# Performance work log

Hardware: AMD Instinct MI355X
Metric: run time of the kernel (lower is better)

Reference implementation:

```python
import jax, jax.numpy as jnp
import numpy as np

N = 50000   # nodes
E = 800000  # edges before self-loops
H = 4       # heads
D = 64      # num_h_feats (per-head out dim of hidden layers)
C = 2       # num_classes
NEG = 0.2   # DGL GATConv leaky_relu negative_slope
EPS = 1e-5  # BatchNorm eps


def setup_inputs() -> dict:
    key = jax.random.key(0)
    ks = jax.random.split(key, 16)
    inp = {}
    inp['feats'] = jax.random.normal(ks[0], (N, 9), jnp.float32)
    inp['W1'] = jax.random.normal(ks[1], (9, H * D), jnp.float32) * 0.1
    inp['al1'] = jax.random.normal(ks[2], (H, D), jnp.float32) * 0.1
    inp['ar1'] = jax.random.normal(ks[3], (H, D), jnp.float32) * 0.1
    inp['b1'] = jnp.zeros((H, D), jnp.float32)
    inp['Wm'] = jax.random.normal(ks[4], (D, H * D), jnp.float32) * 0.1
    inp['alm'] = jax.random.normal(ks[5], (H, D), jnp.float32) * 0.1
    inp['arm'] = jax.random.normal(ks[6], (H, D), jnp.float32) * 0.1
    inp['bm'] = jnp.zeros((H, D), jnp.float32)
    inp['W2'] = jax.random.normal(ks[7], (D, H * C), jnp.float32) * 0.1
    inp['al2'] = jax.random.normal(ks[8], (H, C), jnp.float32) * 0.1
    inp['ar2'] = jax.random.normal(ks[9], (H, C), jnp.float32) * 0.1
    inp['b2'] = jnp.zeros((H, C), jnp.float32)
    inp['gamma'] = jnp.ones((D,), jnp.float32)
    inp['beta'] = jnp.zeros((D,), jnp.float32)
    inp['src'] = jax.random.randint(ks[10], (E,), 0, N, jnp.int32)
    inp['dst'] = jax.random.randint(ks[11], (E,), 0, N, jnp.int32)
    return inp


def gat_layer(x, W, al, ar, b, src, dst, out_d):
    """DGL GATConv: linear -> per-edge attention -> dst-softmax -> scatter-sum."""
    n = x.shape[0]
    z = (x @ W).reshape(n, H, out_d)                 # [N, H, Dout]
    el = jnp.sum(z * al, axis=-1)                    # [N, H] attn on src
    er = jnp.sum(z * ar, axis=-1)                    # [N, H] attn on dst
    e = jax.nn.leaky_relu(el[src] + er[dst], NEG)    # [E, H]
    m = jax.ops.segment_max(e, dst, num_segments=n)  # per-dst max (stable softmax)
    a = jnp.exp(e - m[dst])
    s = jax.ops.segment_sum(a, dst, num_segments=n)
    alpha = a / s[dst]                               # [E, H]
    out = jax.ops.segment_sum(alpha[:, :, None] * z[src], dst, num_segments=n)
    return out + b                                   # [N, H, Dout]


def batchnorm(h, gamma, beta):
    mu = jnp.mean(h, axis=0)
    var = jnp.var(h, axis=0)
    return (h - mu) * jax.lax.rsqrt(var + EPS) * gamma + beta


def reference(feats, W1, al1, ar1, b1, Wm, alm, arm, bm, W2, al2, ar2, b2,
              gamma, beta, src, dst):
    # dgl.add_self_loop
    loop = jnp.arange(N, dtype=src.dtype)
    s = jnp.concatenate([src, loop])
    d = jnp.concatenate([dst, loop])
    h = gat_layer(feats, W1, al1, ar1, b1, s, d, D).sum(axis=1)  # head-sum
    h = batchnorm(h, gamma, beta)
    h = gat_layer(h, Wm, alm, arm, bm, s, d, D).sum(axis=1)
    h = batchnorm(h, gamma, beta)
    o = gat_layer(h, W2, al2, ar2, b2, s, d, C).sum(axis=1)      # [N, C]
    return o
```

## Files before the change

kernel.cpp:

```cpp
#include <hip/hip_runtime.h>
#include <hip/hip_bf16.h>

typedef __hip_bfloat16 bf16;
typedef __bf16 bf16x8 __attribute__((ext_vector_type(8)));
typedef float f32x4 __attribute__((ext_vector_type(4)));
typedef _Float16 h16;
typedef _Float16 h16x4 __attribute__((ext_vector_type(4)));

#define LOG2E 1.44269504088896340736f

__device__ __forceinline__ float b2f(bf16 v) { return __bfloat162float(v); }

__device__ __forceinline__ float ldin(const void* p, size_t i, int isb) {
    return isb ? b2f(((const bf16*)p)[i]) : ((const float*)p)[i];
}
__device__ __forceinline__ unsigned short f2bfbits(float f) {
    bf16 v = __float2bfloat16(f);
    return *(unsigned short*)&v;
}

__global__ __launch_bounds__(256) void prep_kernel(
    const void* __restrict__ feats, const void* __restrict__ W1, const void* __restrict__ Wm,
    const void* __restrict__ al1, const void* __restrict__ ar1,
    const void* __restrict__ alm, const void* __restrict__ arm,
    const unsigned* __restrict__ gbits,
    unsigned short* __restrict__ fpad, unsigned short* __restrict__ W1T,
    unsigned short* __restrict__ WmT,
    float* __restrict__ alf1, float* __restrict__ arf1,
    float* __restrict__ alfm, float* __restrict__ arfm,
    unsigned short* __restrict__ zhs, float* __restrict__ zcs, float* __restrict__ elp,
    int* __restrict__ flag, int Nn) {
    int isb = (gbits[0] == 0x3F803F80u) ? 1 : 0;
    long t = (long)blockIdx.x * 256 + threadIdx.x;
    if (t == 0) *flag = isb;
    long n64 = (long)Nn * 64;
    if (t < n64) {
        int k = (int)(t & 63); long n = t >> 6;
        fpad[t] = (k < 9) ? f2bfbits(ldin(feats, (size_t)n * 9 + k, isb)) : 0;
    } else if (t < n64 + 16384) {
        long u = t - n64; int n = (int)(u >> 6), k = (int)(u & 63);
        W1T[u] = (k < 9) ? f2bfbits(ldin(W1, (size_t)k * 256 + n, isb)) : 0;
    } else if (t < n64 + 32768) {
        long u = t - n64 - 16384; int n = (int)(u >> 6), k = (int)(u & 63);
        WmT[u] = f2bfbits(ldin(Wm, (size_t)k * 256 + n, isb));
    } else if (t < n64 + 32768 + 256) {
        int u = (int)(t - n64 - 32768);
        alf1[u] = ldin(al1, u, isb) * LOG2E; arf1[u] = ldin(ar1, u, isb) * LOG2E;
        alfm[u] = ldin(alm, u, isb) * LOG2E; arfm[u] = ldin(arm, u, isb) * LOG2E;
    } else {
        long u = t - (n64 + 32768 + 256);
        if (u < 4) {
            elp[(size_t)Nn * 4 + u] = -1e30f;
        } else if (u < 260) {
            zhs[(size_t)Nn * 256 + (u - 4)] = 0;
        } else if (u < 268) {
            zcs[(size_t)Nn * 8 + (u - 260)] = 0.f;
        }
    }
}

__global__ __launch_bounds__(256) void count_kernel(
    const int* __restrict__ dst, int* __restrict__ deg, int E) {
    int t = blockIdx.x * 256 + threadIdx.x;
    if (t < E) atomicAdd(&deg[dst[t]], 1);
}

__global__ __launch_bounds__(256) void scan1_kernel(
    const int* __restrict__ deg, int* __restrict__ off, int* __restrict__ bsum, int Nn) {
    __shared__ int s[256];
    int t = threadIdx.x, i = blockIdx.x * 256 + t;
    int v = (i < Nn) ? deg[i] : 0;
    s[t] = v; __syncthreads();
#pragma unroll
    for (int o = 1; o < 256; o <<= 1) {
        int a = (t >= o) ? s[t - o] : 0;
        __syncthreads();
        s[t] += a;
        __syncthreads();
    }
    if (i < Nn) off[i] = s[t];
    if (t == 255) bsum[blockIdx.x] = s[255];
}

__global__ __launch_bounds__(256) void scan2_kernel(int* __restrict__ bsum, int NB) {
    __shared__ int s[256];
    int t = threadIdx.x;
    int v = (t < NB) ? bsum[t] : 0;
    s[t] = v; __syncthreads();
#pragma unroll
    for (int o = 1; o < 256; o <<= 1) {
        int a = (t >= o) ? s[t - o] : 0;
        __syncthreads();
        s[t] += a;
        __syncthreads();
    }
    if (t < NB) bsum[t] = s[t] - v;
}

__global__ __launch_bounds__(256) void scan3_kernel(
    const int* __restrict__ deg, int* __restrict__ off, int* __restrict__ cur,
    const int* __restrict__ bsum, int Nn, int E) {
    int i = blockIdx.x * 256 + threadIdx.x;
    if (i < Nn) {
        int ex = off[i] - deg[i] + bsum[i >> 8];
        off[i] = ex;
        cur[i] = ex;
    }
    if (i == 0) off[Nn] = E;
}

__global__ __launch_bounds__(256) void scatter_kernel(
    const int* __restrict__ src, const int* __restrict__ dst,
    int* __restrict__ cur, int* __restrict__ adj, int E) {
    int t = blockIdx.x * 256 + threadIdx.x;
    if (t < E) {
        int p = atomicAdd(&cur[dst[t]], 1);
        adj[p] = src[t];
    }
}

__global__ __launch_bounds__(256) void lin_mfma_l1_kernel(
    const unsigned short* __restrict__ xb, const unsigned short* __restrict__ WT,
    const float* __restrict__ alf, const float* __restrict__ arf,
    h16* __restrict__ zh, float* __restrict__ el, float* __restrict__ er, int Nn) {
    __shared__ h16 zs[16 * 256];
    int w = threadIdx.x >> 6;
    int l = threadIdx.x & 63;
    int quad = l >> 4, lc = l & 15;
    int node0 = blockIdx.x * 16;

    int mrow = node0 + lc; if (mrow >= Nn) mrow = Nn - 1;
    const bf16x8* xa = (const bf16x8*)(xb + (size_t)mrow * 64);
    bf16x8 a0 = xa[quad];
    bf16x8 a1 = xa[quad + 4];

    float pe[4] = {0.f, 0.f, 0.f, 0.f}, pr[4] = {0.f, 0.f, 0.f, 0.f};
    int row0 = quad * 4;
#pragma unroll
    for (int ct = 0; ct < 4; ++ct) {
        int col = w * 64 + ct * 16 + lc;
        const bf16x8* wb = (const bf16x8*)(WT + (size_t)col * 64);
        bf16x8 b0 = wb[quad];
        bf16x8 b1 = wb[quad + 4];
        f32x4 c = {0.f, 0.f, 0.f, 0.f};
        c = __builtin_amdgcn_mfma_f32_16x16x32_bf16(a0, b0, c, 0, 0, 0);
        c = __builtin_amdgcn_mfma_f32_16x16x32_bf16(a1, b1, c, 0, 0, 0);
        float av = alf[col], rv = arf[col];
#pragma unroll
        for (int r = 0; r < 4; ++r) {
            pe[r] = fmaf(c[r], av, pe[r]);
            pr[r] = fmaf(c[r], rv, pr[r]);
            zs[(row0 + r) * 256 + col] = (h16)c[r];
        }
    }
#pragma unroll
    for (int o = 1; o < 16; o <<= 1) {
#pragma unroll
        for (int r = 0; r < 4; ++r) {
            pe[r] += __shfl_xor(pe[r], o);
            pr[r] += __shfl_xor(pr[r], o);
        }
    }
    if (lc == 0) {
#pragma unroll
        for (int r = 0; r < 4; ++r) {
            int n = node0 + row0 + r;
            if (n < Nn) { el[n * 4 + w] = pe[r]; er[n * 4 + w] = pr[r]; }
        }
    }
    __syncthreads();
#pragma unroll
    for (int it = 0; it < 2; ++it) {
        int flat = it * 2048 + threadIdx.x * 8;
        int row = flat >> 8;
        if (node0 + row < Nn)
            *(uint4*)(zh + (size_t)node0 * 256 + flat) = *(const uint4*)(zs + flat);
    }
}

__global__ __launch_bounds__(256) void lin_mfma_bn_kernel(
    const float* __restrict__ x, const float* __restrict__ sc, const float* __restrict__ shb,
    const unsigned short* __restrict__ WT,
    const float* __restrict__ alf, const float* __restrict__ arf,
    h16* __restrict__ zh, float* __restrict__ el, float* __restrict__ er, int Nn) {
    __shared__ h16 zs[16 * 256];
    int w = threadIdx.x >> 6;
    int l = threadIdx.x & 63;
    int quad = l >> 4, lc = l & 15;
    int node0 = blockIdx.x * 16;

    int mrow = node0 + lc; if (mrow >= Nn) mrow = Nn - 1;
    const float* xr = x + (size_t)mrow * 64 + quad * 8;
    float4 f0 = ((const float4*)xr)[0];
    float4 f1 = ((const float4*)xr)[1];
    float4 f2 = ((const float4*)(xr + 32))[0];
    float4 f3 = ((const float4*)(xr + 32))[1];
    float4 s0 = ((const float4*)(sc + quad * 8))[0];
    float4 s1 = ((const float4*)(sc + quad * 8))[1];
    float4 s2 = ((const float4*)(sc + 32 + quad * 8))[0];
    float4 s3 = ((const float4*)(sc + 32 + quad * 8))[1];
    float4 h0 = ((const float4*)(shb + quad * 8))[0];
    float4 h1 = ((const float4*)(shb + quad * 8))[1];
    float4 h2 = ((const float4*)(shb + 32 + quad * 8))[0];
    float4 h3 = ((const float4*)(shb + 32 + quad * 8))[1];

    union { bf16x8 v; unsigned short s[8]; } ua, ub;
    ua.s[0] = f2bfbits(fmaf(f0.x, s0.x, h0.x));
    ua.s[1] = f2bfbits(fmaf(f0.y, s0.y, h0.y));
    ua.s[2] = f2bfbits(fmaf(f0.z, s0.z, h0.z));
    ua.s[3] = f2bfbits(fmaf(f0.w, s0.w, h0.w));
    ua.s[4] = f2bfbits(fmaf(f1.x, s1.x, h1.x));
    ua.s[5] = f2bfbits(fmaf(f1.y, s1.y, h1.y));
    ua.s[6] = f2bfbits(fmaf(f1.z, s1.z, h1.z));
    ua.s[7] = f2bfbits(fmaf(f1.w, s1.w, h1.w));
    ub.s[0] = f2bfbits(fmaf(f2.x, s2.x, h2.x));
    ub.s[1] = f2bfbits(fmaf(f2.y, s2.y, h2.y));
    ub.s[2] = f2bfbits(fmaf(f2.z, s2.z, h2.z));
    ub.s[3] = f2bfbits(fmaf(f2.w, s2.w, h2.w));
    ub.s[4] = f2bfbits(fmaf(f3.x, s3.x, h3.x));
    ub.s[5] = f2bfbits(fmaf(f3.y, s3.y, h3.y));
    ub.s[6] = f2bfbits(fmaf(f3.z, s3.z, h3.z));
    ub.s[7] = f2bfbits(fmaf(f3.w, s3.w, h3.w));
    bf16x8 a0 = ua.v, a1 = ub.v;

    float pe[4] = {0.f, 0.f, 0.f, 0.f}, pr[4] = {0.f, 0.f, 0.f, 0.f};
    int row0 = quad * 4;
#pragma unroll
    for (int ct = 0; ct < 4; ++ct) {
        int col = w * 64 + ct * 16 + lc;
        const bf16x8* wb = (const bf16x8*)(WT + (size_t)col * 64);
        bf16x8 b0 = wb[quad];
        bf16x8 b1 = wb[quad + 4];
        f32x4 c = {0.f, 0.f, 0.f, 0.f};
        c = __builtin_amdgcn_mfma_f32_16x16x32_bf16(a0, b0, c, 0, 0, 0);
        c = __builtin_amdgcn_mfma_f32_16x16x32_bf16(a1, b1, c, 0, 0, 0);
        float av = alf[col], rv = arf[col];
#pragma unroll
        for (int r = 0; r < 4; ++r) {
            pe[r] = fmaf(c[r], av, pe[r]);
            pr[r] = fmaf(c[r], rv, pr[r]);
            zs[(row0 + r) * 256 + col] = (h16)c[r];
        }
    }
#pragma unroll
    for (int o = 1; o < 16; o <<= 1) {
#pragma unroll
        for (int r = 0; r < 4; ++r) {
            pe[r] += __shfl_xor(pe[r], o);
            pr[r] += __shfl_xor(pr[r], o);
        }
    }
    if (lc == 0) {
#pragma unroll
        for (int r = 0; r < 4; ++r) {
            int n = node0 + row0 + r;
            if (n < Nn) { el[n * 4 + w] = pe[r]; er[n * 4 + w] = pr[r]; }
        }
    }
    __syncthreads();
#pragma unroll
    for (int it = 0; it < 2; ++it) {
        int flat = it * 2048 + threadIdx.x * 8;
        int row = flat >> 8;
        if (node0 + row < Nn)
            *(uint4*)(zh + (size_t)node0 * 256 + flat) = *(const uint4*)(zs + flat);
    }
}

__global__ __launch_bounds__(256) void bnstats_kernel(
    const float* __restrict__ x, float* __restrict__ bnsum, float* __restrict__ bnsumsq,
    int Nn) {
    __shared__ float ssum[4][64], ssq[4][64];
    int tid = threadIdx.x;
    int d = tid & 63, r = tid >> 6;
    float s = 0.f, q = 0.f;
    int stride = gridDim.x * 4;
    for (int n = blockIdx.x * 4 + r; n < Nn; n += stride) {
        float v = x[(size_t)n * 64 + d];
        s += v;
        q = fmaf(v, v, q);
    }
    ssum[r][d] = s; ssq[r][d] = q;
    __syncthreads();
    if (tid < 64) {
        float ts = ssum[0][tid] + ssum[1][tid] + ssum[2][tid] + ssum[3][tid];
        float tq = ssq[0][tid] + ssq[1][tid] + ssq[2][tid] + ssq[3][tid];
        atomicAdd(&bnsum[tid], ts);
        atomicAdd(&bnsumsq[tid], tq);
    }
}

__global__ void bn_coef_kernel(
    const float* __restrict__ bnsum, const float* __restrict__ bnsumsq,
    const void* __restrict__ gamma, const void* __restrict__ beta,
    float* __restrict__ sc, float* __restrict__ shb,
    const int* __restrict__ flag, int Nn) {
    int isb = *flag;
    int d = threadIdx.x;
    if (d >= 64) return;
    float inv_n = 1.f / (float)Nn;
    float mu = bnsum[d] * inv_n;
    float var = bnsumsq[d] * inv_n - mu * mu;
    float s = rsqrtf(var + 1e-5f) * ldin(gamma, d, isb);
    sc[d] = s;
    shb[d] = ldin(beta, d, isb) - mu * s;
}

__global__ __launch_bounds__(256) void lin3_kernel(
    const float* __restrict__ x, const float* __restrict__ sc, const float* __restrict__ shb,
    const void* __restrict__ W, const void* __restrict__ al, const void* __restrict__ ar,
    float* __restrict__ zc, float* __restrict__ el, float* __restrict__ er,
    const int* __restrict__ flag, int Nn) {
    int isb = *flag;
    int t = blockIdx.x * 256 + threadIdx.x;
    if (t >= Nn * 4) return;
    int n = t >> 2, h = t & 3;
    const float* xr = x + (size_t)n * 64;
    float a0 = 0.f, a1 = 0.f;
#pragma unroll 8
    for (int k = 0; k < 64; k++) {
        float xn = fmaf(xr[k], sc[k], shb[k]);
        a0 += xn * ldin(W, k * 8 + h * 2 + 0, isb);
        a1 += xn * ldin(W, k * 8 + h * 2 + 1, isb);
    }
    zc[n * 8 + h * 2 + 0] = a0;
    zc[n * 8 + h * 2 + 1] = a1;
    el[t] = (a0 * ldin(al, h * 2, isb) + a1 * ldin(al, h * 2 + 1, isb)) * LOG2E;
    er[t] = (a0 * ldin(ar, h * 2, isb) + a1 * ldin(ar, h * 2 + 1, isb)) * LOG2E;
}

#define LDADJ(dstv, bidx)                                   \
    {                                                       \
        _Pragma("unroll") for (int j = 0; j < 4; j++) {     \
            int idx = (bidx) + j;                           \
            int ok = idx < s1;                              \
            int v = adj[ok ? idx : s0];                     \
            dstv[j] = ok ? v : Nn;                          \
        }                                                   \
    }
#define ISSUE(ev, zv, ss)                                                          \
    {                                                                              \
        _Pragma("unroll") for (int j = 0; j < 4; j++) ev[j] = el[ss[j] * 4 + h];   \
        _Pragma("unroll") for (int j = 0; j < 4; j++)                              \
            zv[j] = zrow[(size_t)ss[j] * 64 + l];                                  \
    }
#define COMPUTE(ev, zv)                                     \
    {                                                       \
        _Pragma("unroll") for (int j = 0; j < 4; j++) {     \
            float e = ev[j] + ern;                          \
            e = fmaxf(e, 0.2f * e);                         \
            float wj = __builtin_amdgcn_exp2f(e);           \
            lsum += wj;                                     \
            acc.x = fmaf(wj, (float)zv[j].x, acc.x);        \
            acc.y = fmaf(wj, (float)zv[j].y, acc.y);        \
            acc.z = fmaf(wj, (float)zv[j].z, acc.z);        \
            acc.w = fmaf(wj, (float)zv[j].w, acc.w);        \
        }                                                   \
    }

__global__ __launch_bounds__(256) void gat_agg64_kernel(
    const h16* __restrict__ zh, const float* __restrict__ el, const float* __restrict__ er,
    const int* __restrict__ off, const int* __restrict__ adj, const void* __restrict__ bias,
    float* __restrict__ x, const int* __restrict__ flag, int Nn, int total_waves) {
    int isb = *flag;
    int tid = threadIdx.x;
    int l = tid & 63;
    int h = l >> 4;
    int gw = blockIdx.x * 4 + (tid >> 6);
    const h16x4* zrow = (const h16x4*)zh;

    float4 bsl;
    bsl.x = ldin(bias, l * 4 + 0, isb);
    bsl.y = ldin(bias, l * 4 + 1, isb);
    bsl.z = ldin(bias, l * 4 + 2, isb);
    bsl.w = ldin(bias, l * 4 + 3, isb);

    if (gw >= Nn) return;

    int n = gw;
    int fs0 = off[n], fs1 = off[n + 1];
    float fel = el[n * 4 + h], fer = er[n * 4 + h];

    while (true) {
        int s0 = fs0, s1 = fs1;
        float eln = fel, ern = fer;
        h16x4 zself = zrow[(size_t)n * 64 + l];
        int nn = n + total_waves;
        if (nn < Nn) {
            fs0 = off[nn]; fs1 = off[nn + 1];
            fel = el[nn * 4 + h]; fer = er[nn * 4 + h];
        }

        float e0 = eln + ern;
        e0 = fmaxf(e0, 0.2f * e0);
        float w0 = __builtin_amdgcn_exp2f(e0);
        float lsum = w0;
        float4 acc = {0.f, 0.f, 0.f, 0.f};

        int deg = s1 - s0;
        if (deg > 0) {
            int nb = (deg + 3) >> 2;
            int sA[4], sB[4];
            float evA[4], evB[4];
            h16x4 zvA[4], zvB[4];
            LDADJ(sA, s0);
            ISSUE(evA, zvA, sA);
            if (nb > 1) LDADJ(sB, s0 + 4);
            int k = 0;
            while (true) {
                if (k + 1 < nb) ISSUE(evB, zvB, sB);
                if (k + 2 < nb) LDADJ(sA, s0 + (k + 2) * 4);
                COMPUTE(evA, zvA);
                if (++k >= nb) break;
                if (k + 1 < nb) ISSUE(evA, zvA, sA);
                if (k + 2 < nb) LDADJ(sB, s0 + (k + 2) * 4);
                COMPUTE(evB, zvB);
                if (++k >= nb) break;
            }
        }

        acc.x = fmaf(w0, (float)zself.x, acc.x);
        acc.y = fmaf(w0, (float)zself.y, acc.y);
        acc.z = fmaf(w0, (float)zself.z, acc.z);
        acc.w = fmaf(w0, (float)zself.w, acc.w);

        float inv = 1.f / lsum;
        float4 r;
        r.x = fmaf(acc.x, inv, bsl.x);
        r.y = fmaf(acc.y, inv, bsl.y);
        r.z = fmaf(acc.z, inv, bsl.z);
        r.w = fmaf(acc.w, inv, bsl.w);
#pragma unroll
        for (int o = 16; o < 64; o <<= 1) {
            r.x += __shfl_xor(r.x, o);
            r.y += __shfl_xor(r.y, o);
            r.z += __shfl_xor(r.z, o);
            r.w += __shfl_xor(r.w, o);
        }
        if (h == 0) ((float4*)(x + (size_t)n * 64))[l & 15] = r;
        if (nn >= Nn) break;
        n = nn;
    }
}
#undef LDADJ
#undef ISSUE
#undef COMPUTE

__global__ __launch_bounds__(256) void gat_agg2_kernel(
    const float* __restrict__ zc, const float* __restrict__ el, const float* __restrict__ er,
    const int* __restrict__ off, const int* __restrict__ adj, const void* __restrict__ bias,
    void* __restrict__ out, const int* __restrict__ flag, int Nn) {
    int isb = *flag;
    int t = blockIdx.x * 256 + threadIdx.x;
    if (t >= Nn * 4) return;
    int n = t >> 2, h = t & 3;
    float er_nh = er[n * 4 + h];
    float e0 = el[n * 4 + h] + er_nh;
    e0 = fmaxf(e0, 0.2f * e0);
    float w0 = __builtin_amdgcn_exp2f(e0);
    float lsum = w0;
    float2 zn = ((const float2*)zc)[n * 4 + h];
    float a0 = w0 * zn.x, a1 = w0 * zn.y;
    int s0 = off[n], s1 = off[n + 1];
    for (int i = s0; i < s1; i += 4) {
        int ss[4];
#pragma unroll
        for (int j = 0; j < 4; j++) {
            int idx = i + j;
            int ok = idx < s1;
            int v = adj[ok ? idx : s0];
            ss[j] = ok ? v : Nn;
        }
        float ev[4]; float2 zj[4];
#pragma unroll
        for (int j = 0; j < 4; j++) {
            ev[j] = el[ss[j] * 4 + h];
            zj[j] = ((const float2*)zc)[ss[j] * 4 + h];
        }
#pragma unroll
        for (int j = 0; j < 4; j++) {
            float e = ev[j] + er_nh;
            e = fmaxf(e, 0.2f * e);
            float w = __builtin_amdgcn_exp2f(e);
            lsum += w;
            a0 = fmaf(w, zj[j].x, a0);
            a1 = fmaf(w, zj[j].y, a1);
        }
    }
    float inv = 1.f / lsum;
    float v0 = fmaf(a0, inv, ldin(bias, h * 2 + 0, isb));
    float v1 = fmaf(a1, inv, ldin(bias, h * 2 + 1, isb));
#pragma unroll
    for (int o = 1; o < 4; o <<= 1) {
        v0 += __shfl_xor(v0, o);
        v1 += __shfl_xor(v1, o);
    }
    if (h == 0) {
        if (isb) {
            ((bf16*)out)[n * 2 + 0] = __float2bfloat16(v0);
            ((bf16*)out)[n * 2 + 1] = __float2bfloat16(v1);
        } else {
            ((float*)out)[n * 2 + 0] = v0;
            ((float*)out)[n * 2 + 1] = v1;
        }
    }
}

extern "C" void kernel_launch(void* const* d_in, const int* in_sizes, int n_in,
                              void* d_out, int out_size, void* d_ws, size_t ws_size,
                              hipStream_t stream) {
    const void* feats = d_in[0];
    const void* W1    = d_in[1];
    const void* al1   = d_in[2];
    const void* ar1   = d_in[3];
    const void* b1    = d_in[4];
    const void* Wm    = d_in[5];
    const void* alm   = d_in[6];
    const void* arm   = d_in[7];
    const void* bm    = d_in[8];
    const void* W2    = d_in[9];
    const void* al2   = d_in[10];
    const void* ar2   = d_in[11];
    const void* b2v   = d_in[12];
    const void* gamma = d_in[13];
    const void* beta  = d_in[14];
    const int*  src   = (const int*)d_in[15];
    const int*  dst   = (const int*)d_in[16];

    int Nn = in_sizes[0] / 9;
    int E  = in_sizes[15];

    float* ws = (float*)d_ws;
    h16*   zh   = (h16*)ws;
    float* zc   = ws + (size_t)Nn * 128 + 128;
    float* el   = zc + (size_t)Nn * 8 + 8;
    float* er   = el + (size_t)Nn * 4 + 4;
    float* x    = er + (size_t)Nn * 4;
    int*   deg  = (int*)(x + (size_t)Nn * 64);
    float* bns1 = (float*)(deg + Nn);
    float* bnq1 = bns1 + 64;
    float* bns2 = bnq1 + 64;
    float* bnq2 = bns2 + 64;
    size_t msetBytes = (size_t)Nn * 4 + 256 * 4;
    float* sc1  = bnq2 + 64;
    float* shb1 = sc1 + 64;
    float* sc2  = shb1 + 64;
    float* shb2 = sc2 + 64;
    float* alf1 = shb2 + 64;
    float* arf1 = alf1 + 256;
    float* alfm = arf1 + 256;
    float* arfm = alfm + 256;
    unsigned short* fpad = (unsigned short*)(arfm + 256);
    unsigned short* W1T  = fpad + (size_t)Nn * 64;
    unsigned short* WmT  = W1T + 256 * 64;
    int*   flag = (int*)(WmT + 256 * 64);
    int*   off  = flag + 1;
    int*   cur  = off + Nn + 1;
    int*   adj  = cur + Nn;
    int*   bsum = adj + E;

    dim3 B(256);
    int NB1 = (Nn + 255) / 256;
    int gE  = (E + 255) / 256;
    int gMF = (Nn + 15) / 16;
    int gN4 = (Nn * 4 + 255) / 256;
    long prepN = (long)Nn * 64 + 32768 + 256 + 268;
    int gPrep = (int)((prepN + 255) / 256);
    int AGG_GRID = 2048;
    int total_waves = AGG_GRID * 4;

    prep_kernel<<<gPrep, B, 0, stream>>>(feats, W1, Wm, al1, ar1, alm, arm,
                                         (const unsigned*)gamma, fpad, W1T, WmT,
                                         alf1, arf1, alfm, arfm,
                                         (unsigned short*)zh, zc, el, flag, Nn);

    hipMemsetAsync(deg, 0, msetBytes, stream);
    count_kernel<<<gE, B, 0, stream>>>(dst, deg, E);
    scan1_kernel<<<NB1, B, 0, stream>>>(deg, off, bsum, Nn);
    scan2_kernel<<<1, B, 0, stream>>>(bsum, NB1);
    scan3_kernel<<<NB1, B, 0, stream>>>(deg, off, cur, bsum, Nn, E);
    scatter_kernel<<<gE, B, 0, stream>>>(src, dst, cur, adj, E);

    lin_mfma_l1_kernel<<<gMF, B, 0, stream>>>(fpad, W1T, alf1, arf1, zh, el, er, Nn);
    gat_agg64_kernel<<<AGG_GRID, B, 0, stream>>>(
        zh, el, er, off, adj, b1, x, flag, Nn, total_waves);
    bnstats_kernel<<<512, B, 0, stream>>>(x, bns1, bnq1, Nn);
    bn_coef_kernel<<<1, 64, 0, stream>>>(bns1, bnq1, gamma, beta, sc1, shb1, flag, Nn);

    lin_mfma_bn_kernel<<<gMF, B, 0, stream>>>(x, sc1, shb1, WmT, alfm, arfm, zh, el, er, Nn);
    gat_agg64_kernel<<<AGG_GRID, B, 0, stream>>>(
        zh, el, er, off, adj, bm, x, flag, Nn, total_waves);
    bnstats_kernel<<<512, B, 0, stream>>>(x, bns2, bnq2, Nn);
    bn_coef_kernel<<<1, 64, 0, stream>>>(bns2, bnq2, gamma, beta, sc2, shb2, flag, Nn);

    lin3_kernel<<<gN4, B, 0, stream>>>(x, sc2, shb2, W2, al2, ar2, zc, el, er, flag, Nn);
    gat_agg2_kernel<<<gN4, B, 0, stream>>>(zc, el, er, off, adj, b2v, d_out, flag, Nn);
}
```

Before: 465.2 us.

## Fuse CSR build and BN coef into neighbors; pad adjacency to 4 for vector loads

Folds the degree count into the prep kernel and replaces the three-kernel scan with a single-block scan that pads each node's neighbor list to a multiple of 4, using sentinel entries that point at the padding node. The aggregation kernels then read neighbors with aligned int4 loads and no bounds masks. BN coefficient computation moves into the consuming linear kernels, and the prep kernel writes 16-byte vectors. This removes several small launches and per-edge masking, at the cost of a serial single-block scan over 50k nodes and some padded edge work.

```diff
diff --git a/kernel.cpp b/kernel.cpp
--- a/kernel.cpp
+++ b/kernel.cpp
@@ -24,53 +24,84 @@
     const void* __restrict__ al1, const void* __restrict__ ar1,
     const void* __restrict__ alm, const void* __restrict__ arm,
     const unsigned* __restrict__ gbits,
+    const int* __restrict__ dstv, int* __restrict__ deg,
     unsigned short* __restrict__ fpad, unsigned short* __restrict__ W1T,
     unsigned short* __restrict__ WmT,
     float* __restrict__ alf1, float* __restrict__ arf1,
     float* __restrict__ alfm, float* __restrict__ arfm,
     unsigned short* __restrict__ zhs, float* __restrict__ zcs, float* __restrict__ elp,
-    int* __restrict__ flag, int Nn) {
+    int* __restrict__ flag, int Nn, int E) {
     int isb = (gbits[0] == 0x3F803F80u) ? 1 : 0;
     long t = (long)blockIdx.x * 256 + threadIdx.x;
     if (t == 0) *flag = isb;
-    long n64 = (long)Nn * 64;
-    if (t < n64) {
-        int k = (int)(t & 63); long n = t >> 6;
-        fpad[t] = (k < 9) ? f2bfbits(ldin(feats, (size_t)n * 9 + k, isb)) : 0;
-    } else if (t < n64 + 16384) {
-        long u = t - n64; int n = (int)(u >> 6), k = (int)(u & 63);
-        W1T[u] = (k < 9) ? f2bfbits(ldin(W1, (size_t)k * 256 + n, isb)) : 0;
-    } else if (t < n64 + 32768) {
-        long u = t - n64 - 16384; int n = (int)(u >> 6), k = (int)(u & 63);
-        WmT[u] = f2bfbits(ldin(Wm, (size_t)k * 256 + n, isb));
-    } else if (t < n64 + 32768 + 256) {
-        int u = (int)(t - n64 - 32768);
+    long b0 = (long)Nn * 8;
+    long b1 = b0 + 2048;
+    long b2 = b1 + 2048;
+    long b3 = b2 + 256;
+    long b4 = b3 + 268;
+    long b5 = b4 + E;
+    if (t < b0) {
+        int s = (int)(t & 7); long n = t >> 3;
+        int k0 = s * 8;
+        union { unsigned short us[8]; uint4 v; } o;
+#pragma unroll
+        for (int j = 0; j < 8; j++) {
+            int k = k0 + j;
+            o.us[j] = (k < 9) ? f2bfbits(ldin(feats, (size_t)n * 9 + k, isb))
+                              : (unsigned short)0;
+        }
+        *(uint4*)(fpad + t * 8) = o.v;
+    } else if (t < b1) {
+        long u = t - b0;
+        int col = (int)(u >> 3), k0 = ((int)u & 7) * 8;
+        union { unsigned short us[8]; uint4 v; } o;
+#pragma unroll
+        for (int j = 0; j < 8; j++) {
+            int k = k0 + j;
+            o.us[j] = (k < 9) ? f2bfbits(ldin(W1, (size_t)k * 256 + col, isb))
+                              : (unsigned short)0;
+        }
+        *(uint4*)(W1T + u * 8) = o.v;
+    } else if (t < b2) {
+        long u = t - b1;
+        int col = (int)(u >> 3), k0 = ((int)u & 7) * 8;
+        union { unsigned short us[8]; uint4 v; } o;
+#pragma unroll
+        for (int j = 0; j < 8; j++) {
+            int k = k0 + j;
+            o.us[j] = f2bfbits(ldin(Wm, (size_t)k * 256 + col, isb));
+        }
+        *(uint4*)(WmT + u * 8) = o.v;
+    } else if (t < b3) {
+        int u = (int)(t - b2);
         alf1[u] = ldin(al1, u, isb) * LOG2E; arf1[u] = ldin(ar1, u, isb) * LOG2E;
         alfm[u] = ldin(alm, u, isb) * LOG2E; arfm[u] = ldin(arm, u, isb) * LOG2E;
-    } else {
-        long u = t - (n64 + 32768 + 256);
+    } else if (t < b4) {
+        long u = t - b3;
         if (u < 4) {
             elp[(size_t)Nn * 4 + u] = -1e30f;
         } else if (u < 260) {
             zhs[(size_t)Nn * 256 + (u - 4)] = 0;
-        } else if (u < 268) {
+        } else {
             zcs[(size_t)Nn * 8 + (u - 260)] = 0.f;
         }
-    }
-}
-
-__global__ __launch_bounds__(256) void count_kernel(
-    const int* __restrict__ dst, int* __restrict__ deg, int E) {
-    int t = blockIdx.x * 256 + threadIdx.x;
-    if (t < E) atomicAdd(&deg[dst[t]], 1);
-}
-
-__global__ __launch_bounds__(256) void scan1_kernel(
-    const int* __restrict__ deg, int* __restrict__ off, int* __restrict__ bsum, int Nn) {
+    } else if (t < b5) {
+        atomicAdd(&deg[dstv[t - b4]], 1);
+    }
+}
+
+__global__ __launch_bounds__(256) void scanpad_kernel(
+    const int* __restrict__ deg, int* __restrict__ off, int* __restrict__ cur,
+    int* __restrict__ adj, int Nn) {
     __shared__ int s[256];
-    int t = threadIdx.x, i = blockIdx.x * 256 + t;
-    int v = (i < Nn) ? deg[i] : 0;
-    s[t] = v; __syncthreads();
+    int t = threadIdx.x;
+    int chunk = (Nn + 255) >> 8;
+    int lo = t * chunk, hi = lo + chunk;
+    if (hi > Nn) hi = Nn;
+    if (lo > Nn) lo = Nn;
+    int sum = 0;
+    for (int i = lo; i < hi; i++) sum += (deg[i] + 3) & ~3;
+    s[t] = sum; __syncthreads();
 #pragma unroll
     for (int o = 1; o < 256; o <<= 1) {
         int a = (t >= o) ? s[t - o] : 0;
@@ -78,35 +109,19 @@
         s[t] += a;
         __syncthreads();
     }
-    if (i < Nn) off[i] = s[t];
-    if (t == 255) bsum[blockIdx.x] = s[255];
-}
-
-__global__ __launch_bounds__(256) void scan2_kernel(int* __restrict__ bsum, int NB) {
-    __shared__ int s[256];
-    int t = threadIdx.x;
-    int v = (t < NB) ? bsum[t] : 0;
-    s[t] = v; __syncthreads();
-#pragma unroll
-    for (int o = 1; o < 256; o <<= 1) {
-        int a = (t >= o) ? s[t - o] : 0;
-        __syncthreads();
-        s[t] += a;
-        __syncthreads();
-    }
-    if (t < NB) bsum[t] = s[t] - v;
-}
-
-__global__ __launch_bounds__(256) void scan3_kernel(
-    const int* __restrict__ deg, int* __restrict__ off, int* __restrict__ cur,
-    const int* __restrict__ bsum, int Nn, int E) {
-    int i = blockIdx.x * 256 + threadIdx.x;
-    if (i < Nn) {
-        int ex = off[i] - deg[i] + bsum[i >> 8];
-        off[i] = ex;
-        cur[i] = ex;
-    }
-    if (i == 0) off[Nn] = E;
+    int run = s[t] - sum;
+    for (int i = lo; i < hi; i++) {
+        int d = deg[i], pd = (d + 3) & ~3;
+        off[i] = run; cur[i] = run;
+        for (int j = d; j < pd; j++) adj[run + j] = Nn;
+        run += pd;
+    }
+    if (t == 255) {
+        int tot = s[255];
+        off[Nn] = tot;
+#pragma unroll
+        for (int j = 0; j < 8; j++) adj[tot + j] = Nn;
+    }
 }
 
 __global__ __launch_bounds__(256) void scatter_kernel(
@@ -179,13 +194,29 @@
 }
 
 __global__ __launch_bounds__(256) void lin_mfma_bn_kernel(
-    const float* __restrict__ x, const float* __restrict__ sc, const float* __restrict__ shb,
+    const float* __restrict__ x,
+    const float* __restrict__ bnsum, const float* __restrict__ bnsumsq,
+    const void* __restrict__ gamma, const void* __restrict__ beta,
     const unsigned short* __restrict__ WT,
     const float* __restrict__ alf, const float* __restrict__ arf,
-    h16* __restrict__ zh, float* __restrict__ el, float* __restrict__ er, int Nn) {
+    h16* __restrict__ zh, float* __restrict__ el, float* __restrict__ er,
+    const int* __restrict__ flag, int Nn) {
     __shared__ h16 zs[16 * 256];
-    int w = threadIdx.x >> 6;
-    int l = threadIdx.x & 63;
+    __shared__ __align__(16) float scs[64], shs[64];
+    int tid = threadIdx.x;
+    if (tid < 64) {
+        int isb = *flag;
+        float inv_n = 1.f / (float)Nn;
+        float mu = bnsum[tid] * inv_n;
+        float var = bnsumsq[tid] * inv_n - mu * mu;
+        float s = rsqrtf(var + 1e-5f) * ldin(gamma, tid, isb);
+        scs[tid] = s;
+        shs[tid] = ldin(beta, tid, isb) - mu * s;
+    }
+    __syncthreads();
+
+    int w = tid >> 6;
+    int l = tid & 63;
     int quad = l >> 4, lc = l & 15;
     int node0 = blockIdx.x * 16;
 
@@ -195,14 +226,14 @@
     float4 f1 = ((const float4*)xr)[1];
     float4 f2 = ((const float4*)(xr + 32))[0];
     float4 f3 = ((const float4*)(xr + 32))[1];
-    float4 s0 = ((const float4*)(sc + quad * 8))[0];
-    float4 s1 = ((const float4*)(sc + quad * 8))[1];
-    float4 s2 = ((const float4*)(sc + 32 + quad * 8))[0];
-    float4 s3 = ((const float4*)(sc + 32 + quad * 8))[1];
-    float4 h0 = ((const float4*)(shb + quad * 8))[0];
-    float4 h1 = ((const float4*)(shb + quad * 8))[1];
-    float4 h2 = ((const float4*)(shb + 32 + quad * 8))[0];
-    float4 h3 = ((const float4*)(shb + 32 + quad * 8))[1];
+    float4 s0 = ((const float4*)(scs + quad * 8))[0];
+    float4 s1 = ((const float4*)(scs + quad * 8))[1];
+    float4 s2 = ((const float4*)(scs + 32 + quad * 8))[0];
+    float4 s3 = ((const float4*)(scs + 32 + quad * 8))[1];
+    float4 h0 = ((const float4*)(shs + quad * 8))[0];
+    float4 h1 = ((const float4*)(shs + quad * 8))[1];
+    float4 h2 = ((const float4*)(shs + 32 + quad * 8))[0];
+    float4 h3 = ((const float4*)(shs + 32 + quad * 8))[1];
 
     union { bf16x8 v; unsigned short s[8]; } ua, ub;
     ua.s[0] = f2bfbits(fmaf(f0.x, s0.x, h0.x));
@@ -290,38 +321,47 @@
     }
 }
 
-__global__ void bn_coef_kernel(
+__global__ __launch_bounds__(256) void lin3_kernel(
+    const float* __restrict__ x,
     const float* __restrict__ bnsum, const float* __restrict__ bnsumsq,
     const void* __restrict__ gamma, const void* __restrict__ beta,
-    float* __restrict__ sc, float* __restrict__ shb,
-    const int* __restrict__ flag, int Nn) {
-    int isb = *flag;
-    int d = threadIdx.x;
-    if (d >= 64) return;
-    float inv_n = 1.f / (float)Nn;
-    float mu = bnsum[d] * inv_n;
-    float var = bnsumsq[d] * inv_n - mu * mu;
-    float s = rsqrtf(var + 1e-5f) * ldin(gamma, d, isb);
-    sc[d] = s;
-    shb[d] = ldin(beta, d, isb) - mu * s;
-}
-
-__global__ __launch_bounds__(256) void lin3_kernel(
-    const float* __restrict__ x, const float* __restrict__ sc, const float* __restrict__ shb,
     const void* __restrict__ W, const void* __restrict__ al, const void* __restrict__ ar,
     float* __restrict__ zc, float* __restrict__ el, float* __restrict__ er,
     const int* __restrict__ flag, int Nn) {
+    __shared__ __align__(16) float scs[64], shs[64];
     int isb = *flag;
-    int t = blockIdx.x * 256 + threadIdx.x;
+    int tid = threadIdx.x;
+    if (tid < 64) {
+        float inv_n = 1.f / (float)Nn;
+        float mu = bnsum[tid] * inv_n;
+        float var = bnsumsq[tid] * inv_n - mu * mu;
+        float s = rsqrtf(var + 1e-5f) * ldin(gamma, tid, isb);
+        scs[tid] = s;
+        shs[tid] = ldin(beta, tid, isb) - mu * s;
+    }
+    __syncthreads();
+    int t = blockIdx.x * 256 + tid;
     if (t >= Nn * 4) return;
     int n = t >> 2, h = t & 3;
-    const float* xr = x + (size_t)n * 64;
+    const float4* xr4 = (const float4*)(x + (size_t)n * 64);
     float a0 = 0.f, a1 = 0.f;
-#pragma unroll 8
-    for (int k = 0; k < 64; k++) {
-        float xn = fmaf(xr[k], sc[k], shb[k]);
-        a0 += xn * ldin(W, k * 8 + h * 2 + 0, isb);
-        a1 += xn * ldin(W, k * 8 + h * 2 + 1, isb);
+#pragma unroll 4
+    for (int kk = 0; kk < 16; kk++) {
+        float4 xv = xr4[kk];
+        int k = kk * 4;
+        float xn;
+        xn = fmaf(xv.x, scs[k + 0], shs[k + 0]);
+        a0 += xn * ldin(W, (k + 0) * 8 + h * 2, isb);
+        a1 += xn * ldin(W, (k + 0) * 8 + h * 2 + 1, isb);
+        xn = fmaf(xv.y, scs[k + 1], shs[k + 1]);
+        a0 += xn * ldin(W, (k + 1) * 8 + h * 2, isb);
+        a1 += xn * ldin(W, (k + 1) * 8 + h * 2 + 1, isb);
+        xn = fmaf(xv.z, scs[k + 2], shs[k + 2]);
+        a0 += xn * ldin(W, (k + 2) * 8 + h * 2, isb);
+        a1 += xn * ldin(W, (k + 2) * 8 + h * 2 + 1, isb);
+        xn = fmaf(xv.w, scs[k + 3], shs[k + 3]);
+        a0 += xn * ldin(W, (k + 3) * 8 + h * 2, isb);
+        a1 += xn * ldin(W, (k + 3) * 8 + h * 2 + 1, isb);
     }
     zc[n * 8 + h * 2 + 0] = a0;
     zc[n * 8 + h * 2 + 1] = a1;
@@ -329,22 +369,16 @@
     er[t] = (a0 * ldin(ar, h * 2, isb) + a1 * ldin(ar, h * 2 + 1, isb)) * LOG2E;
 }
 
-#define LDADJ(dstv, bidx)                                   \
-    {                                                       \
-        _Pragma("unroll") for (int j = 0; j < 4; j++) {     \
-            int idx = (bidx) + j;                           \
-            int ok = idx < s1;                              \
-            int v = adj[ok ? idx : s0];                     \
-            dstv[j] = ok ? v : Nn;                          \
-        }                                                   \
-    }
-#define ISSUE(ev, zv, ss)                                                          \
-    {                                                                              \
-        _Pragma("unroll") for (int j = 0; j < 4; j++) ev[j] = el[ss[j] * 4 + h];   \
-        _Pragma("unroll") for (int j = 0; j < 4; j++)                              \
-            zv[j] = zrow[(size_t)ss[j] * 64 + l];                                  \
-    }
-#define COMPUTE(ev, zv)                                     \
+#define GATH(ev, zv, sv)                                        \
+    {                                                           \
+        ev[0] = el[sv.x * 4 + h]; ev[1] = el[sv.y * 4 + h];     \
+        ev[2] = el[sv.z * 4 + h]; ev[3] = el[sv.w * 4 + h];     \
+        zv[0] = zrow[(size_t)sv.x * 64 + l];                    \
+        zv[1] = zrow[(size_t)sv.y * 64 + l];                    \
+        zv[2] = zrow[(size_t)sv.z * 64 + l];                    \
+        zv[3] = zrow[(size_t)sv.w * 64 + l];                    \
+    }
+#define COMP(ev, zv)                                        \
     {                                                       \
         _Pragma("unroll") for (int j = 0; j < 4; j++) {     \
             float e = ev[j] + ern;                          \
@@ -380,15 +414,19 @@
     int n = gw;
     int fs0 = off[n], fs1 = off[n + 1];
     float fel = el[n * 4 + h], fer = er[n * 4 + h];
+    int4 fsv = *(const int4*)(adj + fs0);
 
     while (true) {
-        int s0 = fs0, s1 = fs1;
+        int s0 = fs0;
+        int nb = (fs1 - fs0) >> 2;
         float eln = fel, ern = fer;
+        int4 svA = fsv;
         h16x4 zself = zrow[(size_t)n * 64 + l];
         int nn = n + total_waves;
         if (nn < Nn) {
             fs0 = off[nn]; fs1 = off[nn + 1];
             fel = el[nn * 4 + h]; fer = er[nn * 4 + h];
+            fsv = *(const int4*)(adj + fs0);
         }
 
         float e0 = eln + ern;
@@ -397,24 +435,20 @@
         float lsum = w0;
         float4 acc = {0.f, 0.f, 0.f, 0.f};
 
-        int deg = s1 - s0;
-        if (deg > 0) {
-            int nb = (deg + 3) >> 2;
-            int sA[4], sB[4];
+        if (nb > 0) {
             float evA[4], evB[4];
             h16x4 zvA[4], zvB[4];
-            LDADJ(sA, s0);
-            ISSUE(evA, zvA, sA);
-            if (nb > 1) LDADJ(sB, s0 + 4);
+            GATH(evA, zvA, svA);
+            int4 svB = *(const int4*)(adj + s0 + 4);
             int k = 0;
             while (true) {
-                if (k + 1 < nb) ISSUE(evB, zvB, sB);
-                if (k + 2 < nb) LDADJ(sA, s0 + (k + 2) * 4);
-                COMPUTE(evA, zvA);
+                if (k + 1 < nb) GATH(evB, zvB, svB);
+                svA = *(const int4*)(adj + s0 + (k + 2) * 4);
+                COMP(evA, zvA);
                 if (++k >= nb) break;
-                if (k + 1 < nb) ISSUE(evA, zvA, sA);
-                if (k + 2 < nb) LDADJ(sB, s0 + (k + 2) * 4);
-                COMPUTE(evB, zvB);
+                if (k + 1 < nb) GATH(evA, zvA, svA);
+                svB = *(const int4*)(adj + s0 + (k + 2) * 4);
+                COMP(evB, zvB);
                 if (++k >= nb) break;
             }
         }
@@ -442,9 +476,8 @@
         n = nn;
     }
 }
-#undef LDADJ
-#undef ISSUE
-#undef COMPUTE
+#undef GATH
+#undef COMP
 
 __global__ __launch_bounds__(256) void gat_agg2_kernel(
     const float* __restrict__ zc, const float* __restrict__ el, const float* __restrict__ er,
@@ -454,29 +487,22 @@
     int t = blockIdx.x * 256 + threadIdx.x;
     if (t >= Nn * 4) return;
     int n = t >> 2, h = t & 3;
+    const float2* zc2 = (const float2*)zc;
     float er_nh = er[n * 4 + h];
     float e0 = el[n * 4 + h] + er_nh;
     e0 = fmaxf(e0, 0.2f * e0);
     float w0 = __builtin_amdgcn_exp2f(e0);
     float lsum = w0;
-    float2 zn = ((const float2*)zc)[n * 4 + h];
+    float2 zn = zc2[n * 4 + h];
     float a0 = w0 * zn.x, a1 = w0 * zn.y;
     int s0 = off[n], s1 = off[n + 1];
     for (int i = s0; i < s1; i += 4) {
-        int ss[4];
-#pragma unroll
-        for (int j = 0; j < 4; j++) {
-            int idx = i + j;
-            int ok = idx < s1;
-            int v = adj[ok ? idx : s0];
-            ss[j] = ok ? v : Nn;
-        }
+        int4 sv = *(const int4*)(adj + i);
         float ev[4]; float2 zj[4];
-#pragma unroll
-        for (int j = 0; j < 4; j++) {
-            ev[j] = el[ss[j] * 4 + h];
-            zj[j] = ((const float2*)zc)[ss[j] * 4 + h];
-        }
+        ev[0] = el[sv.x * 4 + h]; zj[0] = zc2[sv.x * 4 + h];
+        ev[1] = el[sv.y * 4 + h]; zj[1] = zc2[sv.y * 4 + h];
+        ev[2] = el[sv.z * 4 + h]; zj[2] = zc2[sv.z * 4 + h];
+        ev[3] = el[sv.w * 4 + h]; zj[3] = zc2[sv.w * 4 + h];
 #pragma unroll
         for (int j = 0; j < 4; j++) {
             float e = ev[j] + er_nh;
@@ -532,7 +558,7 @@
 
     float* ws = (float*)d_ws;
     h16*   zh   = (h16*)ws;
-    float* zc   = ws + (size_t)Nn * 128 + 128;
+    float* zc   = ws + (size_t)(Nn + 1) * 128;
     float* el   = zc + (size_t)Nn * 8 + 8;
     float* er   = el + (size_t)Nn * 4 + 4;
     float* x    = er + (size_t)Nn * 4;
@@ -542,57 +568,51 @@
     float* bns2 = bnq1 + 64;
     float* bnq2 = bns2 + 64;
     size_t msetBytes = (size_t)Nn * 4 + 256 * 4;
-    float* sc1  = bnq2 + 64;
-    float* shb1 = sc1 + 64;
-    float* sc2  = shb1 + 64;
-    float* shb2 = sc2 + 64;
-    float* alf1 = shb2 + 64;
+    float* alf1 = bnq2 + 64;
     float* arf1 = alf1 + 256;
     float* alfm = arf1 + 256;
     float* arfm = alfm + 256;
-    unsigned short* fpad = (unsigned short*)(arfm + 256);
+    unsigned short* fpad =
+        (unsigned short*)(((uintptr_t)(arfm + 256) + 15) & ~(uintptr_t)15);
     unsigned short* W1T  = fpad + (size_t)Nn * 64;
     unsigned short* WmT  = W1T + 256 * 64;
     int*   flag = (int*)(WmT + 256 * 64);
     int*   off  = flag + 1;
     int*   cur  = off + Nn + 1;
-    int*   adj  = cur + Nn;
-    int*   bsum = adj + E;
+    int*   adj  = (int*)(((uintptr_t)(cur + Nn) + 15) & ~(uintptr_t)15);
 
     dim3 B(256);
-    int NB1 = (Nn + 255) / 256;
     int gE  = (E + 255) / 256;
     int gMF = (Nn + 15) / 16;
     int gN4 = (Nn * 4 + 255) / 256;
-    long prepN = (long)Nn * 64 + 32768 + 256 + 268;
+    long prepN = (long)Nn * 8 + 2048 + 2048 + 256 + 268 + E;
     int gPrep = (int)((prepN + 255) / 256);
     int AGG_GRID = 2048;
     int total_waves = AGG_GRID * 4;
 
+    hipMemsetAsync(deg, 0, msetBytes, stream);
+
     prep_kernel<<<gPrep, B, 0, stream>>>(feats, W1, Wm, al1, ar1, alm, arm,
-                                         (const unsigned*)gamma, fpad, W1T, WmT,
+                                         (const unsigned*)gamma, dst, deg,
+                                         fpad, W1T, WmT,
                                          alf1, arf1, alfm, arfm,
-                                         (unsigned short*)zh, zc, el, flag, Nn);
-
-    hipMemsetAsync(deg, 0, msetBytes, stream);
-    count_kernel<<<gE, B, 0, stream>>>(dst, deg, E);
-    scan1_kernel<<<NB1, B, 0, stream>>>(deg, off, bsum, Nn);
-    scan2_kernel<<<1, B, 0, stream>>>(bsum, NB1);
-    scan3_kernel<<<NB1, B, 0, stream>>>(deg, off, cur, bsum, Nn, E);
+                                         (unsigned short*)zh, zc, el, flag, Nn, E);
+
+    scanpad_kernel<<<1, B, 0, stream>>>(deg, off, cur, adj, Nn);
     scatter_kernel<<<gE, B, 0, stream>>>(src, dst, cur, adj, E);
 
     lin_mfma_l1_kernel<<<gMF, B, 0, stream>>>(fpad, W1T, alf1, arf1, zh, el, er, Nn);
     gat_agg64_kernel<<<AGG_GRID, B, 0, stream>>>(
         zh, el, er, off, adj, b1, x, flag, Nn, total_waves);
     bnstats_kernel<<<512, B, 0, stream>>>(x, bns1, bnq1, Nn);
-    bn_coef_kernel<<<1, 64, 0, stream>>>(bns1, bnq1, gamma, beta, sc1, shb1, flag, Nn);
-
-    lin_mfma_bn_kernel<<<gMF, B, 0, stream>>>(x, sc1, shb1, WmT, alfm, arfm, zh, el, er, Nn);
+
+    lin_mfma_bn_kernel<<<gMF, B, 0, stream>>>(x, bns1, bnq1, gamma, beta,
+                                              WmT, alfm, arfm, zh, el, er, flag, Nn);
     gat_agg64_kernel<<<AGG_GRID, B, 0, stream>>>(
         zh, el, er, off, adj, bm, x, flag, Nn, total_waves);
     bnstats_kernel<<<512, B, 0, stream>>>(x, bns2, bnq2, Nn);
-    bn_coef_kernel<<<1, 64, 0, stream>>>(bns2, bnq2, gamma, beta, sc2, shb2, flag, Nn);
-
-    lin3_kernel<<<gN4, B, 0, stream>>>(x, sc2, shb2, W2, al2, ar2, zc, el, er, flag, Nn);
+
+    lin3_kernel<<<gN4, B, 0, stream>>>(x, bns2, bnq2, gamma, beta,
+                                       W2, al2, ar2, zc, el, er, flag, Nn);
     gat_agg2_kernel<<<gN4, B, 0, stream>>>(zc, el, er, off, adj, b2v, d_out, flag, Nn);
 }
```

Measured after the change: 590.6 us. +27.0%, slower.
